# Performance work log

Hardware: AMD Instinct MI355X
Metric: run time of the kernel (lower is better)

Reference implementation:

```python
import jax, jax.numpy as jnp
import numpy as np

INPUT_SIZE = 1024
HIDDEN_SIZE = 1024
BATCH = 8192
MLP_H1, MLP_H2 = 16, 8


def _uniform(key, shape, stdv):
    return jax.random.uniform(key, shape, jnp.float32, -stdv, stdv)


def setup_inputs() -> dict:
    key = jax.random.key(0)
    ks = jax.random.split(key, 20)
    stdv = 1.0 / np.sqrt(HIDDEN_SIZE)
    I, H = INPUT_SIZE, HIDDEN_SIZE
    inp = {
        "x": jax.random.normal(ks[0], (BATCH, I), jnp.float32),
        "h": jax.random.normal(ks[1], (BATCH, H), jnp.float32),
        "c": jax.random.normal(ks[2], (BATCH, H), jnp.float32),
        # gate weights (torch layout: matmul(h, W_h*) + matmul(x, W_x*) + b)
        "W_hi": _uniform(ks[3], (H, H), stdv),
        "W_xi": _uniform(ks[4], (I, H), stdv),
        "b_i": _uniform(ks[5], (H,), stdv),
        "W_hc": _uniform(ks[6], (H, H), stdv),
        "W_xc": _uniform(ks[7], (I, H), stdv),
        "b_c": _uniform(ks[8], (H,), stdv),
        "W_ho": _uniform(ks[9], (H, H), stdv),
        "W_xo": _uniform(ks[10], (I, H), stdv),
        "b_o": _uniform(ks[11], (H,), stdv),
        # forget MLP: (I+H) -> 16 -> 8 -> H, ReLU hidden, sigmoid output
        "W1": _uniform(ks[12], (I + H, MLP_H1), stdv),
        "b1": _uniform(ks[13], (MLP_H1,), stdv),
        "W2": _uniform(ks[14], (MLP_H1, MLP_H2), stdv),
        "b2": _uniform(ks[15], (MLP_H2,), stdv),
        "W3": _uniform(ks[16], (MLP_H2, H), stdv),
        "b3": _uniform(ks[17], (H,), stdv),
    }
    return inp


def reference(x, h, c, W_hi, W_xi, b_i, W_hc, W_xc, b_c, W_ho, W_xo, b_o,
              W1, b1, W2, b2, W3, b3):
    # forget gate via small MLP on concat(x, h)
    xh = jnp.concatenate((x, h), axis=1)           # [B, I+H]
    z = jax.nn.relu(xh @ W1 + b1)                  # [B, 16]
    z = jax.nn.relu(z @ W2 + b2)                   # [B, 8]
    f = jax.nn.sigmoid(z @ W3 + b3)                # [B, H]

    i = jax.nn.sigmoid(h @ W_hi + x @ W_xi + b_i)
    g = jnp.tanh(h @ W_hc + x @ W_xc + b_c)
    o = jax.nn.sigmoid(h @ W_ho + x @ W_xo + b_o)

    c_new = f * c + i * g
    h_new = o * jnp.tanh(c_new)
    return (h_new, c_new, f)
```

## Files before the change

kernel.cpp:

```cpp
#include <hip/hip_runtime.h>
#include <math.h>

#define BATCH 8192
#define HDIM  1024
#define KDIM  2048
#define NDIM  3072

typedef __attribute__((ext_vector_type(8))) short short8;
typedef __attribute__((ext_vector_type(4))) float floatx4;

__device__ __forceinline__ float b2f(unsigned short u) {
  union { unsigned int i; float f; } v; v.i = ((unsigned int)u) << 16; return v.f;
}
__device__ __forceinline__ unsigned short f2b(float f) {
  union { unsigned int i; float f; } v; v.f = f;
  unsigned int r = v.i + 0x7FFFu + ((v.i >> 16) & 1u);
  return (unsigned short)(r >> 16);
}
__device__ __forceinline__ float ldsel(const void* p, size_t i, int isbf) {
  return isbf ? b2f(((const unsigned short*)p)[i]) : ((const float*)p)[i];
}
__device__ __forceinline__ float sigf(float x) { return 1.0f / (1.0f + __expf(-x)); }
__device__ __forceinline__ float tanhfast(float x) {
  float a = __builtin_fabsf(x);
  float t = __expf(-2.f * a);
  float r = (1.f - t) / (1.f + t);
  return copysignf(r, x);
}

__device__ __forceinline__ void gld16(const void* g, void* l) {
  auto gp = reinterpret_cast<__attribute__((address_space(1))) unsigned int*>(
      (unsigned long long)g);
  auto lp = reinterpret_cast<__attribute__((address_space(3))) unsigned int*>(
      (unsigned long long)l);
  __builtin_amdgcn_global_load_lds(gp, lp, 16, 0, 0);
}

__global__ void k_detect(const unsigned int* __restrict__ x, int* __restrict__ flag) {
  unsigned int w = x[threadIdx.x];
  unsigned short lo = (unsigned short)(w & 0xFFFFu);
  int e = (lo >> 7) & 0xFF;
  bool ok = (e >= 110 && e <= 135) || ((lo & 0x7FFFu) == 0);
  unsigned long long m = __ballot(ok);
  if (threadIdx.x == 0) *flag = (__popcll(m) >= 48) ? 1 : 0;
}

__global__ __launch_bounds__(256) void k_pack_w(
    const void* __restrict__ wxi, const void* __restrict__ whi,
    const void* __restrict__ wxc, const void* __restrict__ whc,
    const void* __restrict__ wxo, const void* __restrict__ who,
    unsigned short* __restrict__ WT, const int* __restrict__ flag) {
  const int isbf = *flag;
  const int bx = blockIdx.x;
  const int mat = bx >> 8;
  const int rem = bx & 255;
  const int ti = rem >> 4;
  const int tj = rem & 15;
  const void* Ws[6] = {wxi, whi, wxc, whc, wxo, who};
  const void* W = Ws[mat];
  const int gt = mat >> 1;
  const int half = mat & 1;
  __shared__ float tbuf[64][65];
  const int t = threadIdx.x;
  const int rrow = t >> 3;
  const int c8 = (t & 7) * 8;
#pragma unroll
  for (int it = 0; it < 2; ++it) {
    int row = it * 32 + rrow;
    size_t off = (size_t)(ti * 64 + row) * 1024 + tj * 64 + c8;
    if (isbf) {
      const unsigned short* s = (const unsigned short*)W + off;
      ushort4 a = *(const ushort4*)(s);
      ushort4 b = *(const ushort4*)(s + 4);
      tbuf[row][c8+0]=b2f(a.x); tbuf[row][c8+1]=b2f(a.y);
      tbuf[row][c8+2]=b2f(a.z); tbuf[row][c8+3]=b2f(a.w);
      tbuf[row][c8+4]=b2f(b.x); tbuf[row][c8+5]=b2f(b.y);
      tbuf[row][c8+6]=b2f(b.z); tbuf[row][c8+7]=b2f(b.w);
    } else {
      const float* s = (const float*)W + off;
      float4 a = *(const float4*)(s);
      float4 b = *(const float4*)(s + 4);
      tbuf[row][c8+0]=a.x; tbuf[row][c8+1]=a.y; tbuf[row][c8+2]=a.z; tbuf[row][c8+3]=a.w;
      tbuf[row][c8+4]=b.x; tbuf[row][c8+5]=b.y; tbuf[row][c8+6]=b.z; tbuf[row][c8+7]=b.w;
    }
  }
  __syncthreads();
#pragma unroll
  for (int it = 0; it < 2; ++it) {
    int nl = it * 32 + rrow;
    int n = gt * 1024 + tj * 64 + nl;
    int kb = half * 1024 + ti * 64 + c8;
    short8 pk;
#pragma unroll
    for (int i = 0; i < 8; ++i) pk[i] = (short)f2b(tbuf[c8 + i][nl]);
    *(short8*)(WT + (size_t)n * KDIM + kb) = pk;
  }
}

__global__ __launch_bounds__(256) void k_pack_small(
    const void* __restrict__ W1, unsigned short* __restrict__ W1T,
    const int* __restrict__ flag) {
  const int isbf = *flag;
  const int t = threadIdx.x;
  for (int k = t; k < 2048; k += 256) {
    unsigned short v[16];
    if (isbf) {
      const unsigned short* r = (const unsigned short*)W1 + (size_t)k * 16;
#pragma unroll
      for (int i = 0; i < 16; ++i) v[i] = r[i];
    } else {
      const float* r = (const float*)W1 + (size_t)k * 16;
#pragma unroll
      for (int i = 0; i < 16; ++i) v[i] = f2b(r[i]);
    }
#pragma unroll
    for (int nn = 0; nn < 16; ++nn) W1T[(size_t)nn * 2048 + k] = v[nn];
  }
}

__global__ __launch_bounds__(256) void k_pack_a(
    const void* __restrict__ x, const void* __restrict__ h,
    unsigned short* __restrict__ A, const int* __restrict__ flag) {
  if (*flag) return;
  size_t idx = ((size_t)blockIdx.x * 256 + threadIdx.x) * 8;
  int k = (int)(idx & 2047);
  size_t m = idx >> 11;
  const float* s = (k < 1024) ? (const float*)x + m * 1024 + k
                              : (const float*)h + m * 1024 + (k - 1024);
  float4 a = *(const float4*)(s);
  float4 b = *(const float4*)(s + 4);
  short8 pk;
  pk[0]=(short)f2b(a.x); pk[1]=(short)f2b(a.y); pk[2]=(short)f2b(a.z); pk[3]=(short)f2b(a.w);
  pk[4]=(short)f2b(b.x); pk[5]=(short)f2b(b.y); pk[6]=(short)f2b(b.z); pk[7]=(short)f2b(b.w);
  *(short8*)(A + idx) = pk;
}

__global__ __launch_bounds__(256, 3) void k_gemm(
    const void* __restrict__ x, const void* __restrict__ h,
    const unsigned short* __restrict__ Apack,
    const unsigned short* __restrict__ WT,
    unsigned short* __restrict__ P, const int* __restrict__ flag) {
  const int isbf = *flag;
  const unsigned short* Ax = isbf ? (const unsigned short*)x : Apack;
  const unsigned short* Ah = isbf ? (const unsigned short*)h : (Apack + 1024);
  const int sA = isbf ? 1024 : 2048;
  __shared__ __align__(16) unsigned short lA[128 * 64];
  __shared__ __align__(16) unsigned short lB[128 * 64];
  const int tid = threadIdx.x;
  const int lane = tid & 63;
  const int wv = tid >> 6;
  const int wm = (wv >> 1) << 6;
  const int wn = (wv & 1) << 6;
  const int m0 = blockIdx.y << 7;
  const int n0 = blockIdx.x << 7;

  floatx4 acc[4][4];
  const floatx4 fzero = {0.f, 0.f, 0.f, 0.f};
#pragma unroll
  for (int i = 0; i < 4; ++i)
#pragma unroll
    for (int j = 0; j < 4; ++j) acc[i][j] = fzero;

  int rr[4], kk[4];
#pragma unroll
  for (int ps = 0; ps < 4; ++ps) {
    int chunk = ps * 256 + tid;
    rr[ps] = chunk >> 3;
    kk[ps] = (chunk & 7) ^ (rr[ps] & 7);
  }
  const int px0 = (lane >> 4) ^ (lane & 7);
  const int px1 = ((lane >> 4) + 4) ^ (lane & 7);
  const int rowA = wm + (lane & 15);
  const int rowB = wn + (lane & 15);

  for (int kt = 0; kt < KDIM / 64; ++kt) {
    const int k0 = kt * 64;
    const unsigned short* Abase = (k0 < 1024) ? (Ax + k0) : (Ah + (k0 - 1024));
#pragma unroll
    for (int ps = 0; ps < 4; ++ps) {
      const int chunk = ps * 256 + tid;
      gld16(Abase + (size_t)(m0 + rr[ps]) * sA + kk[ps] * 8, lA + chunk * 8);
      gld16(WT + ((size_t)(n0 + rr[ps]) * KDIM + k0 + kk[ps] * 8), lB + chunk * 8);
    }
    __syncthreads();
#pragma unroll
    for (int s = 0; s < 2; ++s) {
      const int px = s ? px1 : px0;
      short8 af[4], bfr[4];
#pragma unroll
      for (int i = 0; i < 4; ++i)
        af[i] = *(const short8*)(lA + ((((rowA + (i << 4)) << 3) + px) << 3));
#pragma unroll
      for (int i = 0; i < 4; ++i)
        bfr[i] = *(const short8*)(lB + ((((rowB + (i << 4)) << 3) + px) << 3));
#pragma unroll
      for (int mi = 0; mi < 4; ++mi)
#pragma unroll
        for (int ni = 0; ni < 4; ++ni)
          acc[mi][ni] = __builtin_amdgcn_mfma_f32_16x16x32_bf16(
              af[mi], bfr[ni], acc[mi][ni], 0, 0, 0);
    }
    __syncthreads();
  }
  const int col = lane & 15;
  const int rq = (lane >> 4) << 2;
#pragma unroll
  for (int mi = 0; mi < 4; ++mi) {
#pragma unroll
    for (int ni = 0; ni < 4; ++ni) {
      const size_t n = (size_t)(n0 + wn + (ni << 4) + col);
#pragma unroll
      for (int t = 0; t < 4; ++t) {
        const size_t m = (size_t)(m0 + wm + (mi << 4) + rq + t);
        P[m * NDIM + n] = f2b(acc[mi][ni][t]);
      }
    }
  }
}

__global__ __launch_bounds__(64) void k_z2(
    const void* __restrict__ x, const void* __restrict__ h,
    const unsigned short* __restrict__ Apack,
    const unsigned short* __restrict__ W1T,
    const void* __restrict__ b1, const void* __restrict__ W2,
    const void* __restrict__ b2, float* __restrict__ z2,
    const int* __restrict__ flag) {
  const int isbf = *flag;
  const unsigned short* Ax = isbf ? (const unsigned short*)x : Apack;
  const unsigned short* Ah = isbf ? (const unsigned short*)h : (Apack + 1024);
  const int sA = isbf ? 1024 : 2048;
  const int lane = threadIdx.x;
  const int m0 = blockIdx.x * 16;
  const int q = lane >> 4;
  const int r = lane & 15;
  floatx4 acc = {0.f, 0.f, 0.f, 0.f};
  const unsigned short* arow0 = Ax + (size_t)(m0 + r) * sA;
  const unsigned short* arow1 = Ah + (size_t)(m0 + r) * sA;
  const unsigned short* brow = W1T + (size_t)r * 2048;
#pragma unroll 4
  for (int kt = 0; kt < 32; ++kt) {
    int k = kt * 32 + q * 8;
    short8 a = *(const short8*)(arow0 + k);
    short8 b = *(const short8*)(brow + k);
    acc = __builtin_amdgcn_mfma_f32_16x16x32_bf16(a, b, acc, 0, 0, 0);
  }
#pragma unroll 4
  for (int kt = 0; kt < 32; ++kt) {
    int k = kt * 32 + q * 8;
    short8 a = *(const short8*)(arow1 + k);
    short8 b = *(const short8*)(brow + 1024 + k);
    acc = __builtin_amdgcn_mfma_f32_16x16x32_bf16(a, b, acc, 0, 0, 0);
  }
  __shared__ float z1s[16][17];
  float b1f = ldsel(b1, (size_t)r, isbf);
#pragma unroll
  for (int t = 0; t < 4; ++t) z1s[q * 4 + t][r] = fmaxf(acc[t] + b1f, 0.f);
  __syncthreads();
  const int row = lane >> 2;
  const int p2 = (lane & 3) * 2;
  float s0 = ldsel(b2, (size_t)p2, isbf);
  float s1 = ldsel(b2, (size_t)p2 + 1, isbf);
#pragma unroll
  for (int nn = 0; nn < 16; ++nn) {
    float z = z1s[row][nn];
    s0 += z * ldsel(W2, (size_t)nn * 8 + p2, isbf);
    s1 += z * ldsel(W2, (size_t)nn * 8 + p2 + 1, isbf);
  }
  float2 o = make_float2(fmaxf(s0, 0.f), fmaxf(s1, 0.f));
  *(float2*)(z2 + (size_t)(m0 + row) * 8 + p2) = o;
}

__global__ __launch_bounds__(256) void k_pointwise(
    const unsigned short* __restrict__ P, const void* __restrict__ cin,
    const void* __restrict__ bi, const void* __restrict__ bc,
    const void* __restrict__ bo, const float* __restrict__ z2,
    const void* __restrict__ W3, const void* __restrict__ b3,
    void* __restrict__ out, const int* __restrict__ flag) {
  const int isbf = *flag;
  const size_t MH = (size_t)BATCH * HDIM;
  const size_t m = blockIdx.x;
  const int n = threadIdx.x * 4;
  const size_t idx = m * 1024 + n;
  const unsigned short* pr = P + m * NDIM + n;
  ushort4 ui = *(const ushort4*)(pr);
  ushort4 ug = *(const ushort4*)(pr + 1024);
  ushort4 uo = *(const ushort4*)(pr + 2048);
  float pi[4] = {b2f(ui.x), b2f(ui.y), b2f(ui.z), b2f(ui.w)};
  float pg[4] = {b2f(ug.x), b2f(ug.y), b2f(ug.z), b2f(ug.w)};
  float po[4] = {b2f(uo.x), b2f(uo.y), b2f(uo.z), b2f(uo.w)};
  float4 za = *(const float4*)(z2 + m * 8);
  float4 zb = *(const float4*)(z2 + m * 8 + 4);
  float zz[8] = {za.x, za.y, za.z, za.w, zb.x, zb.y, zb.z, zb.w};
  float f3[4];
  float bif[4], bcf[4], bof[4], cf[4];
  if (isbf) {
    ushort4 u3 = *(const ushort4*)((const unsigned short*)b3 + n);
    f3[0]=b2f(u3.x); f3[1]=b2f(u3.y); f3[2]=b2f(u3.z); f3[3]=b2f(u3.w);
#pragma unroll
    for (int j = 0; j < 8; ++j) {
      ushort4 w = *(const ushort4*)((const unsigned short*)W3 + (size_t)j * 1024 + n);
      f3[0] += zz[j]*b2f(w.x); f3[1] += zz[j]*b2f(w.y);
      f3[2] += zz[j]*b2f(w.z); f3[3] += zz[j]*b2f(w.w);
    }
    ushort4 a = *(const ushort4*)((const unsigned short*)bi + n);
    ushort4 b = *(const ushort4*)((const unsigned short*)bc + n);
    ushort4 d = *(const ushort4*)((const unsigned short*)bo + n);
    ushort4 e = *(const ushort4*)((const unsigned short*)cin + idx);
    bif[0]=b2f(a.x); bif[1]=b2f(a.y); bif[2]=b2f(a.z); bif[3]=b2f(a.w);
    bcf[0]=b2f(b.x); bcf[1]=b2f(b.y); bcf[2]=b2f(b.z); bcf[3]=b2f(b.w);
    bof[0]=b2f(d.x); bof[1]=b2f(d.y); bof[2]=b2f(d.z); bof[3]=b2f(d.w);
    cf[0]=b2f(e.x);  cf[1]=b2f(e.y);  cf[2]=b2f(e.z);  cf[3]=b2f(e.w);
  } else {
    float4 u3 = *(const float4*)((const float*)b3 + n);
    f3[0]=u3.x; f3[1]=u3.y; f3[2]=u3.z; f3[3]=u3.w;
#pragma unroll
    for (int j = 0; j < 8; ++j) {
      float4 w = *(const float4*)((const float*)W3 + (size_t)j * 1024 + n);
      f3[0] += zz[j]*w.x; f3[1] += zz[j]*w.y; f3[2] += zz[j]*w.z; f3[3] += zz[j]*w.w;
    }
    float4 a = *(const float4*)((const float*)bi + n);
    float4 b = *(const float4*)((const float*)bc + n);
    float4 d = *(const float4*)((const float*)bo + n);
    float4 e = *(const float4*)((const float*)cin + idx);
    bif[0]=a.x; bif[1]=a.y; bif[2]=a.z; bif[3]=a.w;
    bcf[0]=b.x; bcf[1]=b.y; bcf[2]=b.z; bcf[3]=b.w;
    bof[0]=d.x; bof[1]=d.y; bof[2]=d.z; bof[3]=d.w;
    cf[0]=e.x;  cf[1]=e.y;  cf[2]=e.z;  cf[3]=e.w;
  }
  float hn[4], cn[4], ff[4];
#pragma unroll
  for (int t = 0; t < 4; ++t) {
    float F = sigf(f3[t]);
    float I = sigf(pi[t] + bif[t]);
    float G = tanhfast(pg[t] + bcf[t]);
    float O = sigf(po[t] + bof[t]);
    float C = F * cf[t] + I * G;
    ff[t] = F;
    cn[t] = C;
    hn[t] = O * tanhfast(C);
  }
  if (isbf) {
    unsigned short* ob = (unsigned short*)out;
    *(ushort4*)(ob + idx) = make_ushort4(f2b(hn[0]), f2b(hn[1]), f2b(hn[2]), f2b(hn[3]));
    *(ushort4*)(ob + MH + idx) = make_ushort4(f2b(cn[0]), f2b(cn[1]), f2b(cn[2]), f2b(cn[3]));
    *(ushort4*)(ob + 2 * MH + idx) = make_ushort4(f2b(ff[0]), f2b(ff[1]), f2b(ff[2]), f2b(ff[3]));
  } else {
    float* ob = (float*)out;
    *(float4*)(ob + idx) = make_float4(hn[0], hn[1], hn[2], hn[3]);
    *(float4*)(ob + MH + idx) = make_float4(cn[0], cn[1], cn[2], cn[3]);
    *(float4*)(ob + 2 * MH + idx) = make_float4(ff[0], ff[1], ff[2], ff[3]);
  }
}

extern "C" void kernel_launch(void* const* d_in, const int* in_sizes, int n_in,
                              void* d_out, int out_size, void* d_ws, size_t ws_size,
                              hipStream_t stream) {
  const void* x    = d_in[0];
  const void* h    = d_in[1];
  const void* c    = d_in[2];
  const void* W_hi = d_in[3];
  const void* W_xi = d_in[4];
  const void* b_i  = d_in[5];
  const void* W_hc = d_in[6];
  const void* W_xc = d_in[7];
  const void* b_c  = d_in[8];
  const void* W_ho = d_in[9];
  const void* W_xo = d_in[10];
  const void* b_o  = d_in[11];
  const void* W1   = d_in[12];
  const void* b1   = d_in[13];
  const void* W2   = d_in[14];
  const void* b2   = d_in[15];
  const void* W3   = d_in[16];
  const void* b3   = d_in[17];

  char* ws = (char*)d_ws;
  unsigned short* A   = (unsigned short*)ws;
  unsigned short* WT  = (unsigned short*)(ws + 33554432);
  unsigned short* P   = (unsigned short*)(ws + 46137344);
  float*          z2b = (float*)(ws + 96468992);
  unsigned short* W1T = (unsigned short*)(ws + 96731136);
  int*           flag = (int*)(ws + 96796672);

  k_detect<<<dim3(1), dim3(64), 0, stream>>>((const unsigned int*)x, flag);
  k_pack_w<<<dim3(6 * 256), dim3(256), 0, stream>>>(W_xi, W_hi, W_xc, W_hc,
                                                    W_xo, W_ho, WT, flag);
  k_pack_small<<<dim3(1), dim3(256), 0, stream>>>(W1, W1T, flag);
  k_pack_a<<<dim3(8192), dim3(256), 0, stream>>>(x, h, A, flag);
  k_gemm<<<dim3(NDIM / 128, BATCH / 128), dim3(256), 0, stream>>>(x, h, A, WT, P, flag);
  k_z2<<<dim3(BATCH / 16), dim3(64), 0, stream>>>(x, h, A, W1T, b1, W2, b2, z2b, flag);
  k_pointwise<<<dim3(BATCH), dim3(256), 0, stream>>>(P, c, b_i, b_c, b_o, z2b,
                                                     W3, b3, d_out, flag);
}
```

Before: 383.5 us.

## Merge packing and MLP kernels into one launch and inline dtype detection

Replaces the detect, weight-pack, W1-pack, A-pack and z2 kernels with one heterogeneous kernel whose block ranges do the MLP first layer, the weight transpose and the activation packing. Every kernel now recomputes the bf16 detection with a wavefront ballot instead of reading a flag. The pointwise kernel stages W3 in shared memory. This cuts launch count and serialization, and in exchange adds a 70KB shared allocation that lowers occupancy for the simple packing blocks and repeats a W3 load in every pointwise block.

```diff
diff --git a/kernel.cpp b/kernel.cpp
--- a/kernel.cpp
+++ b/kernel.cpp
@@ -28,6 +28,15 @@
   return copysignf(r, x);
 }
 
+__device__ __forceinline__ int detect_bf(const void* x) {
+  unsigned int w = ((const unsigned int*)x)[threadIdx.x & 63];
+  unsigned short lo = (unsigned short)(w & 0xFFFFu);
+  int e = (lo >> 7) & 0xFF;
+  bool ok = (e >= 110 && e <= 135) || ((lo & 0x7FFFu) == 0);
+  unsigned long long m = __ballot(ok);
+  return (__popcll(m) >= 48) ? 1 : 0;
+}
+
 __device__ __forceinline__ void gld16(const void* g, void* l) {
   auto gp = reinterpret_cast<__attribute__((address_space(1))) unsigned int*>(
       (unsigned long long)g);
@@ -36,111 +45,166 @@
   __builtin_amdgcn_global_load_lds(gp, lp, 16, 0, 0);
 }
 
-__global__ void k_detect(const unsigned int* __restrict__ x, int* __restrict__ flag) {
-  unsigned int w = x[threadIdx.x];
-  unsigned short lo = (unsigned short)(w & 0xFFFFu);
-  int e = (lo >> 7) & 0xFF;
-  bool ok = (e >= 110 && e <= 135) || ((lo & 0x7FFFu) == 0);
-  unsigned long long m = __ballot(ok);
-  if (threadIdx.x == 0) *flag = (__popcll(m) >= 48) ? 1 : 0;
-}
-
-__global__ __launch_bounds__(256) void k_pack_w(
+__device__ __forceinline__ short8 ld8bf(const void* p, size_t off, int isbf) {
+  short8 r;
+  if (isbf) {
+    r = *(const short8*)((const unsigned short*)p + off);
+  } else {
+    const float* s = (const float*)p + off;
+    float4 a = *(const float4*)(s);
+    float4 b = *(const float4*)(s + 4);
+    r[0]=(short)f2b(a.x); r[1]=(short)f2b(a.y); r[2]=(short)f2b(a.z); r[3]=(short)f2b(a.w);
+    r[4]=(short)f2b(b.x); r[5]=(short)f2b(b.y); r[6]=(short)f2b(b.z); r[7]=(short)f2b(b.w);
+  }
+  return r;
+}
+
+__global__ __launch_bounds__(256) void k_all(
+    const void* __restrict__ x, const void* __restrict__ h,
     const void* __restrict__ wxi, const void* __restrict__ whi,
     const void* __restrict__ wxc, const void* __restrict__ whc,
     const void* __restrict__ wxo, const void* __restrict__ who,
-    unsigned short* __restrict__ WT, const int* __restrict__ flag) {
-  const int isbf = *flag;
+    const void* __restrict__ W1, const void* __restrict__ b1,
+    const void* __restrict__ W2, const void* __restrict__ b2,
+    unsigned short* __restrict__ WT, unsigned short* __restrict__ A,
+    float* __restrict__ z2) {
+  __shared__ __align__(16) char smem[70976];
+  const int isbf = detect_bf(x);
   const int bx = blockIdx.x;
-  const int mat = bx >> 8;
-  const int rem = bx & 255;
-  const int ti = rem >> 4;
-  const int tj = rem & 15;
-  const void* Ws[6] = {wxi, whi, wxc, whc, wxo, who};
-  const void* W = Ws[mat];
-  const int gt = mat >> 1;
-  const int half = mat & 1;
-  __shared__ float tbuf[64][65];
-  const int t = threadIdx.x;
-  const int rrow = t >> 3;
-  const int c8 = (t & 7) * 8;
-#pragma unroll
-  for (int it = 0; it < 2; ++it) {
-    int row = it * 32 + rrow;
-    size_t off = (size_t)(ti * 64 + row) * 1024 + tj * 64 + c8;
-    if (isbf) {
-      const unsigned short* s = (const unsigned short*)W + off;
-      ushort4 a = *(const ushort4*)(s);
-      ushort4 b = *(const ushort4*)(s + 4);
-      tbuf[row][c8+0]=b2f(a.x); tbuf[row][c8+1]=b2f(a.y);
-      tbuf[row][c8+2]=b2f(a.z); tbuf[row][c8+3]=b2f(a.w);
-      tbuf[row][c8+4]=b2f(b.x); tbuf[row][c8+5]=b2f(b.y);
-      tbuf[row][c8+6]=b2f(b.z); tbuf[row][c8+7]=b2f(b.w);
-    } else {
-      const float* s = (const float*)W + off;
-      float4 a = *(const float4*)(s);
-      float4 b = *(const float4*)(s + 4);
-      tbuf[row][c8+0]=a.x; tbuf[row][c8+1]=a.y; tbuf[row][c8+2]=a.z; tbuf[row][c8+3]=a.w;
-      tbuf[row][c8+4]=b.x; tbuf[row][c8+5]=b.y; tbuf[row][c8+6]=b.z; tbuf[row][c8+7]=b.w;
-    }
-  }
-  __syncthreads();
-#pragma unroll
-  for (int it = 0; it < 2; ++it) {
-    int nl = it * 32 + rrow;
-    int n = gt * 1024 + tj * 64 + nl;
-    int kb = half * 1024 + ti * 64 + c8;
+  const int tid = threadIdx.x;
+
+  if (bx < 512) {
+    unsigned short* lW = (unsigned short*)smem;
+    float* part = (float*)(smem + 65536);
+    float* z1s  = (float*)(smem + 69888);
+    const int m0 = bx * 16;
+#pragma unroll
+    for (int it = 0; it < 16; ++it) {
+      const int chunk = it * 256 + tid;
+      const int k = chunk >> 1;
+      const int jh = (chunk & 1) * 8;
+      unsigned short v[8];
+      if (isbf) {
+        short8 s = *(const short8*)((const unsigned short*)W1 + (size_t)k * 16 + jh);
+#pragma unroll
+        for (int j = 0; j < 8; ++j) v[j] = (unsigned short)s[j];
+      } else {
+        const float* s = (const float*)W1 + (size_t)k * 16 + jh;
+        float4 a = *(const float4*)(s);
+        float4 b = *(const float4*)(s + 4);
+        v[0]=f2b(a.x); v[1]=f2b(a.y); v[2]=f2b(a.z); v[3]=f2b(a.w);
+        v[4]=f2b(b.x); v[5]=f2b(b.y); v[6]=f2b(b.z); v[7]=f2b(b.w);
+      }
+#pragma unroll
+      for (int j = 0; j < 8; ++j) {
+        const int row = jh + j;
+        lW[row * 2048 + (((k >> 3) ^ (row & 7)) << 3) + (k & 7)] = v[j];
+      }
+    }
+    __syncthreads();
+    const int w = tid >> 6;
+    const int lane = tid & 63;
+    const int q = lane >> 4;
+    const int r = lane & 15;
+    const void* src = (w >> 1) ? h : x;
+    const size_t abase = (size_t)(m0 + r) * 1024 + (w & 1) * 512;
+    const int kb = (w >> 1) * 1024 + (w & 1) * 512;
+    floatx4 acc = {0.f, 0.f, 0.f, 0.f};
+#pragma unroll 4
+    for (int kt = 0; kt < 16; ++kt) {
+      const int kl = kt * 32 + q * 8;
+      short8 a = ld8bf(src, abase + kl, isbf);
+      const int kg = kb + kl;
+      short8 b = *(const short8*)(lW + r * 2048 + (((kg >> 3) ^ (r & 7)) << 3));
+      acc = __builtin_amdgcn_mfma_f32_16x16x32_bf16(a, b, acc, 0, 0, 0);
+    }
+#pragma unroll
+    for (int t = 0; t < 4; ++t) part[(w * 16 + q * 4 + t) * 17 + r] = acc[t];
+    __syncthreads();
+    {
+      const int row = tid >> 4;
+      const int n = tid & 15;
+      float s = part[(0 * 16 + row) * 17 + n] + part[(1 * 16 + row) * 17 + n] +
+                part[(2 * 16 + row) * 17 + n] + part[(3 * 16 + row) * 17 + n] +
+                ldsel(b1, (size_t)n, isbf);
+      z1s[row * 17 + n] = fmaxf(s, 0.f);
+    }
+    __syncthreads();
+    if (tid < 128) {
+      const int row = tid >> 3;
+      const int p = tid & 7;
+      float s = ldsel(b2, (size_t)p, isbf);
+#pragma unroll
+      for (int nn = 0; nn < 16; ++nn)
+        s += z1s[row * 17 + nn] * ldsel(W2, (size_t)nn * 8 + p, isbf);
+      z2[(size_t)(m0 + row) * 8 + p] = fmaxf(s, 0.f);
+    }
+  } else if (bx < 2048) {
+    float (*tbuf)[65] = (float(*)[65])smem;
+    const int b = bx - 512;
+    const int mat = b >> 8;
+    const int rem = b & 255;
+    const int ti = rem >> 4;
+    const int tj = rem & 15;
+    const void* Ws[6] = {wxi, whi, wxc, whc, wxo, who};
+    const void* W = Ws[mat];
+    const int gt = mat >> 1;
+    const int half = mat & 1;
+    const int rrow = tid >> 3;
+    const int c8 = (tid & 7) * 8;
+#pragma unroll
+    for (int it = 0; it < 2; ++it) {
+      int row = it * 32 + rrow;
+      size_t off = (size_t)(ti * 64 + row) * 1024 + tj * 64 + c8;
+      if (isbf) {
+        const unsigned short* s = (const unsigned short*)W + off;
+        ushort4 a = *(const ushort4*)(s);
+        ushort4 bv = *(const ushort4*)(s + 4);
+        tbuf[row][c8+0]=b2f(a.x);  tbuf[row][c8+1]=b2f(a.y);
+        tbuf[row][c8+2]=b2f(a.z);  tbuf[row][c8+3]=b2f(a.w);
+        tbuf[row][c8+4]=b2f(bv.x); tbuf[row][c8+5]=b2f(bv.y);
+        tbuf[row][c8+6]=b2f(bv.z); tbuf[row][c8+7]=b2f(bv.w);
+      } else {
+        const float* s = (const float*)W + off;
+        float4 a = *(const float4*)(s);
+        float4 bv = *(const float4*)(s + 4);
+        tbuf[row][c8+0]=a.x;  tbuf[row][c8+1]=a.y;  tbuf[row][c8+2]=a.z;  tbuf[row][c8+3]=a.w;
+        tbuf[row][c8+4]=bv.x; tbuf[row][c8+5]=bv.y; tbuf[row][c8+6]=bv.z; tbuf[row][c8+7]=bv.w;
+      }
+    }
+    __syncthreads();
+#pragma unroll
+    for (int it = 0; it < 2; ++it) {
+      int nl = it * 32 + rrow;
+      int n = gt * 1024 + tj * 64 + nl;
+      int kk = half * 1024 + ti * 64 + c8;
+      short8 pk;
+#pragma unroll
+      for (int i = 0; i < 8; ++i) pk[i] = (short)f2b(tbuf[c8 + i][nl]);
+      *(short8*)(WT + (size_t)n * KDIM + kk) = pk;
+    }
+  } else {
+    if (isbf) return;
+    size_t idx = ((size_t)(bx - 2048) * 256 + tid) * 8;
+    int k = (int)(idx & 2047);
+    size_t m = idx >> 11;
+    const float* s = (k < 1024) ? (const float*)x + m * 1024 + k
+                                : (const float*)h + m * 1024 + (k - 1024);
+    float4 a = *(const float4*)(s);
+    float4 b = *(const float4*)(s + 4);
     short8 pk;
-#pragma unroll
-    for (int i = 0; i < 8; ++i) pk[i] = (short)f2b(tbuf[c8 + i][nl]);
-    *(short8*)(WT + (size_t)n * KDIM + kb) = pk;
-  }
-}
-
-__global__ __launch_bounds__(256) void k_pack_small(
-    const void* __restrict__ W1, unsigned short* __restrict__ W1T,
-    const int* __restrict__ flag) {
-  const int isbf = *flag;
-  const int t = threadIdx.x;
-  for (int k = t; k < 2048; k += 256) {
-    unsigned short v[16];
-    if (isbf) {
-      const unsigned short* r = (const unsigned short*)W1 + (size_t)k * 16;
-#pragma unroll
-      for (int i = 0; i < 16; ++i) v[i] = r[i];
-    } else {
-      const float* r = (const float*)W1 + (size_t)k * 16;
-#pragma unroll
-      for (int i = 0; i < 16; ++i) v[i] = f2b(r[i]);
-    }
-#pragma unroll
-    for (int nn = 0; nn < 16; ++nn) W1T[(size_t)nn * 2048 + k] = v[nn];
-  }
-}
-
-__global__ __launch_bounds__(256) void k_pack_a(
-    const void* __restrict__ x, const void* __restrict__ h,
-    unsigned short* __restrict__ A, const int* __restrict__ flag) {
-  if (*flag) return;
-  size_t idx = ((size_t)blockIdx.x * 256 + threadIdx.x) * 8;
-  int k = (int)(idx & 2047);
-  size_t m = idx >> 11;
-  const float* s = (k < 1024) ? (const float*)x + m * 1024 + k
-                              : (const float*)h + m * 1024 + (k - 1024);
-  float4 a = *(const float4*)(s);
-  float4 b = *(const float4*)(s + 4);
-  short8 pk;
-  pk[0]=(short)f2b(a.x); pk[1]=(short)f2b(a.y); pk[2]=(short)f2b(a.z); pk[3]=(short)f2b(a.w);
-  pk[4]=(short)f2b(b.x); pk[5]=(short)f2b(b.y); pk[6]=(short)f2b(b.z); pk[7]=(short)f2b(b.w);
-  *(short8*)(A + idx) = pk;
+    pk[0]=(short)f2b(a.x); pk[1]=(short)f2b(a.y); pk[2]=(short)f2b(a.z); pk[3]=(short)f2b(a.w);
+    pk[4]=(short)f2b(b.x); pk[5]=(short)f2b(b.y); pk[6]=(short)f2b(b.z); pk[7]=(short)f2b(b.w);
+    *(short8*)(A + idx) = pk;
+  }
 }
 
 __global__ __launch_bounds__(256, 3) void k_gemm(
     const void* __restrict__ x, const void* __restrict__ h,
     const unsigned short* __restrict__ Apack,
     const unsigned short* __restrict__ WT,
-    unsigned short* __restrict__ P, const int* __restrict__ flag) {
-  const int isbf = *flag;
+    unsigned short* __restrict__ P) {
+  const int isbf = detect_bf(x);
   const unsigned short* Ax = isbf ? (const unsigned short*)x : Apack;
   const unsigned short* Ah = isbf ? (const unsigned short*)h : (Apack + 1024);
   const int sA = isbf ? 1024 : 2048;
@@ -218,68 +282,35 @@
   }
 }
 
-__global__ __launch_bounds__(64) void k_z2(
-    const void* __restrict__ x, const void* __restrict__ h,
-    const unsigned short* __restrict__ Apack,
-    const unsigned short* __restrict__ W1T,
-    const void* __restrict__ b1, const void* __restrict__ W2,
-    const void* __restrict__ b2, float* __restrict__ z2,
-    const int* __restrict__ flag) {
-  const int isbf = *flag;
-  const unsigned short* Ax = isbf ? (const unsigned short*)x : Apack;
-  const unsigned short* Ah = isbf ? (const unsigned short*)h : (Apack + 1024);
-  const int sA = isbf ? 1024 : 2048;
-  const int lane = threadIdx.x;
-  const int m0 = blockIdx.x * 16;
-  const int q = lane >> 4;
-  const int r = lane & 15;
-  floatx4 acc = {0.f, 0.f, 0.f, 0.f};
-  const unsigned short* arow0 = Ax + (size_t)(m0 + r) * sA;
-  const unsigned short* arow1 = Ah + (size_t)(m0 + r) * sA;
-  const unsigned short* brow = W1T + (size_t)r * 2048;
-#pragma unroll 4
-  for (int kt = 0; kt < 32; ++kt) {
-    int k = kt * 32 + q * 8;
-    short8 a = *(const short8*)(arow0 + k);
-    short8 b = *(const short8*)(brow + k);
-    acc = __builtin_amdgcn_mfma_f32_16x16x32_bf16(a, b, acc, 0, 0, 0);
-  }
-#pragma unroll 4
-  for (int kt = 0; kt < 32; ++kt) {
-    int k = kt * 32 + q * 8;
-    short8 a = *(const short8*)(arow1 + k);
-    short8 b = *(const short8*)(brow + 1024 + k);
-    acc = __builtin_amdgcn_mfma_f32_16x16x32_bf16(a, b, acc, 0, 0, 0);
-  }
-  __shared__ float z1s[16][17];
-  float b1f = ldsel(b1, (size_t)r, isbf);
-#pragma unroll
-  for (int t = 0; t < 4; ++t) z1s[q * 4 + t][r] = fmaxf(acc[t] + b1f, 0.f);
-  __syncthreads();
-  const int row = lane >> 2;
-  const int p2 = (lane & 3) * 2;
-  float s0 = ldsel(b2, (size_t)p2, isbf);
-  float s1 = ldsel(b2, (size_t)p2 + 1, isbf);
-#pragma unroll
-  for (int nn = 0; nn < 16; ++nn) {
-    float z = z1s[row][nn];
-    s0 += z * ldsel(W2, (size_t)nn * 8 + p2, isbf);
-    s1 += z * ldsel(W2, (size_t)nn * 8 + p2 + 1, isbf);
-  }
-  float2 o = make_float2(fmaxf(s0, 0.f), fmaxf(s1, 0.f));
-  *(float2*)(z2 + (size_t)(m0 + row) * 8 + p2) = o;
-}
-
 __global__ __launch_bounds__(256) void k_pointwise(
-    const unsigned short* __restrict__ P, const void* __restrict__ cin,
+    const unsigned short* __restrict__ P, const void* __restrict__ x,
+    const void* __restrict__ cin,
     const void* __restrict__ bi, const void* __restrict__ bc,
     const void* __restrict__ bo, const float* __restrict__ z2,
     const void* __restrict__ W3, const void* __restrict__ b3,
-    void* __restrict__ out, const int* __restrict__ flag) {
-  const int isbf = *flag;
+    void* __restrict__ out) {
+  const int isbf = detect_bf(x);
+  __shared__ unsigned short w3s[8192];
+  const int tid = threadIdx.x;
+#pragma unroll
+  for (int it = 0; it < 4; ++it) {
+    const int idx = (it * 256 + tid) * 8;
+    if (isbf) {
+      *(short8*)(w3s + idx) = *(const short8*)((const unsigned short*)W3 + idx);
+    } else {
+      const float* s = (const float*)W3 + idx;
+      float4 a = *(const float4*)(s);
+      float4 b = *(const float4*)(s + 4);
+      short8 pk;
+      pk[0]=(short)f2b(a.x); pk[1]=(short)f2b(a.y); pk[2]=(short)f2b(a.z); pk[3]=(short)f2b(a.w);
+      pk[4]=(short)f2b(b.x); pk[5]=(short)f2b(b.y); pk[6]=(short)f2b(b.z); pk[7]=(short)f2b(b.w);
+      *(short8*)(w3s + idx) = pk;
+    }
+  }
+  __syncthreads();
   const size_t MH = (size_t)BATCH * HDIM;
   const size_t m = blockIdx.x;
-  const int n = threadIdx.x * 4;
+  const int n = tid * 4;
   const size_t idx = m * 1024 + n;
   const unsigned short* pr = P + m * NDIM + n;
   ushort4 ui = *(const ushort4*)(pr);
@@ -296,12 +327,6 @@
   if (isbf) {
     ushort4 u3 = *(const ushort4*)((const unsigned short*)b3 + n);
     f3[0]=b2f(u3.x); f3[1]=b2f(u3.y); f3[2]=b2f(u3.z); f3[3]=b2f(u3.w);
-#pragma unroll
-    for (int j = 0; j < 8; ++j) {
-      ushort4 w = *(const ushort4*)((const unsigned short*)W3 + (size_t)j * 1024 + n);
-      f3[0] += zz[j]*b2f(w.x); f3[1] += zz[j]*b2f(w.y);
-      f3[2] += zz[j]*b2f(w.z); f3[3] += zz[j]*b2f(w.w);
-    }
     ushort4 a = *(const ushort4*)((const unsigned short*)bi + n);
     ushort4 b = *(const ushort4*)((const unsigned short*)bc + n);
     ushort4 d = *(const ushort4*)((const unsigned short*)bo + n);
@@ -313,11 +338,6 @@
   } else {
     float4 u3 = *(const float4*)((const float*)b3 + n);
     f3[0]=u3.x; f3[1]=u3.y; f3[2]=u3.z; f3[3]=u3.w;
-#pragma unroll
-    for (int j = 0; j < 8; ++j) {
-      float4 w = *(const float4*)((const float*)W3 + (size_t)j * 1024 + n);
-      f3[0] += zz[j]*w.x; f3[1] += zz[j]*w.y; f3[2] += zz[j]*w.z; f3[3] += zz[j]*w.w;
-    }
     float4 a = *(const float4*)((const float*)bi + n);
     float4 b = *(const float4*)((const float*)bc + n);
     float4 d = *(const float4*)((const float*)bo + n);
@@ -326,6 +346,14 @@
     bcf[0]=b.x; bcf[1]=b.y; bcf[2]=b.z; bcf[3]=b.w;
     bof[0]=d.x; bof[1]=d.y; bof[2]=d.z; bof[3]=d.w;
     cf[0]=e.x;  cf[1]=e.y;  cf[2]=e.z;  cf[3]=e.w;
+  }
+#pragma unroll
+  for (int j = 0; j < 8; ++j) {
+    const unsigned short* wr = w3s + j * 1024 + n;
+    f3[0] += zz[j] * b2f(wr[0]);
+    f3[1] += zz[j] * b2f(wr[1]);
+    f3[2] += zz[j] * b2f(wr[2]);
+    f3[3] += zz[j] * b2f(wr[3]);
   }
   float hn[4], cn[4], ff[4];
 #pragma unroll
@@ -379,16 +407,11 @@
   unsigned short* WT  = (unsigned short*)(ws + 33554432);
   unsigned short* P   = (unsigned short*)(ws + 46137344);
   float*          z2b = (float*)(ws + 96468992);
-  unsigned short* W1T = (unsigned short*)(ws + 96731136);
-  int*           flag = (int*)(ws + 96796672);
-
-  k_detect<<<dim3(1), dim3(64), 0, stream>>>((const unsigned int*)x, flag);
-  k_pack_w<<<dim3(6 * 256), dim3(256), 0, stream>>>(W_xi, W_hi, W_xc, W_hc,
-                                                    W_xo, W_ho, WT, flag);
-  k_pack_small<<<dim3(1), dim3(256), 0, stream>>>(W1, W1T, flag);
-  k_pack_a<<<dim3(8192), dim3(256), 0, stream>>>(x, h, A, flag);
-  k_gemm<<<dim3(NDIM / 128, BATCH / 128), dim3(256), 0, stream>>>(x, h, A, WT, P, flag);
-  k_z2<<<dim3(BATCH / 16), dim3(64), 0, stream>>>(x, h, A, W1T, b1, W2, b2, z2b, flag);
-  k_pointwise<<<dim3(BATCH), dim3(256), 0, stream>>>(P, c, b_i, b_c, b_o, z2b,
-                                                     W3, b3, d_out, flag);
-}
+
+  k_all<<<dim3(512 + 1536 + 8192), dim3(256), 0, stream>>>(
+      x, h, W_xi, W_hi, W_xc, W_hc, W_xo, W_ho, W1, b_i ? b1 : b1, W2, b2,
+      WT, A, z2b);
+  k_gemm<<<dim3(NDIM / 128, BATCH / 128), dim3(256), 0, stream>>>(x, h, A, WT, P);
+  k_pointwise<<<dim3(BATCH), dim3(256), 0, stream>>>(P, x, c, b_i, b_c, b_o,
+                                                     z2b, W3, b3, d_out);
+}
```

Measured after the change: 374.2 us. -2.4%, faster.
